# Optimization experiments

Measured on AMD Instinct MI355X. Metric: run time of the kernel, lower is better.

## Reference

```python
import jax, jax.numpy as jnp
import numpy as np

N = 40000; E = 400000; F = 16; H = 8; C = 64; R1 = 40; R2 = 40; MAXR = 60
NEG_SLOPE = 0.2


def setup_inputs() -> dict:
    key = jax.random.key(0)
    ks = jax.random.split(key, 16)
    inp = {}
    inp['x1'] = jax.random.normal(ks[0], (N, F), dtype=jnp.float32)
    inp['edge_index1'] = jax.random.randint(ks[1], (2, E), 0, N)
    inp['edge_attr1'] = jax.random.normal(ks[2], (E, 4), dtype=jnp.float32)
    inp['route_vec1'] = jax.random.randint(ks[3], (N,), 0, R1)
    inp['n_routes1'] = R1
    inp['x2'] = jax.random.normal(ks[4], (N, F), dtype=jnp.float32)
    inp['edge_index2'] = jax.random.randint(ks[5], (2, E), 0, N)
    inp['edge_attr2'] = jax.random.normal(ks[6], (E, 4), dtype=jnp.float32)
    inp['route_vec2'] = jax.random.randint(ks[7], (N,), 0, R2)
    inp['n_routes2'] = R2
    # GATConv params (glorot-ish scaling)
    inp['W_gat'] = jax.random.normal(ks[8], (F, H * C), dtype=jnp.float32) / np.sqrt(F)
    inp['att_src'] = jax.random.normal(ks[9], (H, C), dtype=jnp.float32) / np.sqrt(C)
    inp['att_dst'] = jax.random.normal(ks[10], (H, C), dtype=jnp.float32) / np.sqrt(C)
    inp['bias_gat'] = jnp.zeros((H * C,), dtype=jnp.float32)
    # route combination head: Linear(2*H*C -> MAXR+1)
    D = 2 * H * C
    inp['W_head'] = jax.random.normal(ks[11], (D, MAXR + 1), dtype=jnp.float32) / np.sqrt(D)
    inp['b_head'] = jnp.zeros((MAXR + 1,), dtype=jnp.float32)
    return inp


def _gat_conv(x, edge_index, W, att_src, att_dst, bias):
    """PyG GATConv (concat=True, add_self_loops=True, eval-mode dropout, edge_attr ignored)."""
    n = x.shape[0]
    loops = jnp.arange(n, dtype=edge_index.dtype)
    ei = jnp.concatenate([edge_index, jnp.stack([loops, loops])], axis=1)
    src, dst = ei[0], ei[1]
    h = (x @ W).reshape(n, H, C)                      # [N,H,C]
    a_s = jnp.sum(h * att_src, axis=-1)               # [N,H]
    a_d = jnp.sum(h * att_dst, axis=-1)               # [N,H]
    e = jax.nn.leaky_relu(a_s[src] + a_d[dst], NEG_SLOPE)   # [E',H]
    m = jax.ops.segment_max(e, dst, num_segments=n)   # stable softmax per dst node
    ex = jnp.exp(e - m[dst])
    denom = jax.ops.segment_sum(ex, dst, num_segments=n)
    alpha = ex / denom[dst]                           # [E',H]
    out = jax.ops.segment_sum(h[src] * alpha[:, :, None], dst, num_segments=n)  # [N,H,C]
    return out.reshape(n, H * C) + bias


def reference(x1, edge_index1, edge_attr1, route_vec1, n_routes1,
              x2, edge_index2, edge_attr2, route_vec2, n_routes2,
              W_gat, att_src, att_dst, bias_gat, W_head, b_head):
    # edge_attr is ignored: GATConv was built without edge_dim.
    emb1 = _gat_conv(x1, edge_index1, W_gat, att_src, att_dst, bias_gat)  # [N,H*C]
    emb2 = _gat_conv(x2, edge_index2, W_gat, att_src, att_dst, bias_gat)
    # one-hot(node->route).T @ emb  ==  segment_sum over routes
    agg1 = jax.ops.segment_sum(emb1, route_vec1, num_segments=n_routes1)  # [R1,H*C]
    agg2 = jax.ops.segment_sum(emb2, route_vec2, num_segments=n_routes2)  # [R2,H*C]
    a = jnp.broadcast_to(agg1[:, None, :], (n_routes1, n_routes2, H * C))
    b = jnp.broadcast_to(agg2[None, :, :], (n_routes1, n_routes2, H * C))
    pair = jnp.concatenate([a, b], axis=-1)                               # [R1,R2,2HC]
    full = pair @ W_head + b_head                                         # [R1,R2,MAXR+1]
    max_to_swap = min(n_routes1, n_routes2)
    logits = full[:n_routes1, :n_routes2, :max_to_swap - 1]
    probs = jax.nn.softmax(logits.reshape(-1), axis=-1).reshape(logits.shape)
    return probs
```

## Files before the change

kernel.cpp:

```cpp
#include <hip/hip_runtime.h>
#include <hip/hip_fp16.h>

#define NN 40000
#define NE 400000
#define NF 16
#define NH 8
#define NR 40
#define NK 39
#define NEG 0.2f
#define NBLK 157
#define NCH 16
#define NB 157
#define SLOT 3328
#define BPG2 196
#define GAB 40
#define WS 0.0625f

#define OFF_AS   0
#define OFF_AD   (OFF_AS + 2*NN*NH)
#define OFF_P    (OFF_AD + 2*NN*NH)
#define OFF_PART (OFF_P + 2*NR*NK)
#define OFF_S    (OFF_PART + 2*NR*NCH*128)
#define OFF_XH   (OFF_S + 2*NN*64)
#define OFF_INT  (OFF_XH + 2*NN*8)
#define IOFF_RHIST  0
#define IOFF_BCUR   (2*NR)
#define IOFF_RCUR   (2*NR + 2*NB)
#define IOFF_START  (IOFF_RCUR + 2*NR)
#define IOFF_DEG    (IOFF_START + 2*NN)
#define IOFF_NID    (IOFF_DEG + 2*NN)
#define IOFF_BINNED (IOFF_NID + 2*NN)
#define IOFF_SRC    (IOFF_BINNED + 2*NB*SLOT)

static __device__ __forceinline__ unsigned int f2bf(float v) {
    unsigned int x = __float_as_uint(v);
    return (x + 0x7FFFu + ((x >> 16) & 1u)) >> 16;
}
static __device__ __forceinline__ float bf2f(unsigned int u) {
    return __uint_as_float(u << 16);
}
static __device__ __forceinline__ unsigned int packh2(float a, float b) {
    __half2 hv = __floats2half2_rn(a, b);
    return *(unsigned int*)&hv;
}
static __device__ __forceinline__ float2 unpackh2(unsigned int u) {
    __half2 hv = *(__half2*)&u;
    return __half22float2(hv);
}

__global__ __launch_bounds__(512) void k_zero(int* __restrict__ p,
                                              int* __restrict__ srcs) {
    int i = threadIdx.x;
    if (i < 2 * NR + 2 * NB + 2 * NR) p[i] = 0;
    if (i == 0) srcs[2 * NB * SLOT] = 0;
}

__global__ __launch_bounds__(1024) void k_front(const float* __restrict__ x1,
                                                const float* __restrict__ x2,
                                                const int* __restrict__ rv1,
                                                const int* __restrict__ rv2,
                                                const int* __restrict__ ei1,
                                                const int* __restrict__ ei2,
                                                const float* __restrict__ W,
                                                const float* __restrict__ asrc,
                                                const float* __restrict__ adst,
                                                float* __restrict__ as_,
                                                float* __restrict__ ad_,
                                                unsigned int* __restrict__ xh,
                                                int* __restrict__ rhist,
                                                int* __restrict__ bcur,
                                                unsigned int* __restrict__ binned) {
    __shared__ float us[256];
    __shared__ int lh[NR];
    __shared__ int lhb[NB], lbb[NB];
    int tid = threadIdx.x;
    if (blockIdx.x < 2 * GAB) {
        if (tid < NR) lh[tid] = 0;
        if (tid < 256) {
            int tt = tid & 127;
            int f = tt >> 3, h = tt & 7;
            const float* av = (tid < 128 ? asrc : adst) + h * 64;
            const float* wrow = W + f * 512 + h * 64;
            float su = 0.f;
            for (int c = 0; c < 64; ++c) su += wrow[c] * av[c];
            us[tid] = su;
        }
        __syncthreads();
        int g = blockIdx.x / GAB;
        int n = (blockIdx.x - g * GAB) * 1024 + tid;
        if (n < NN) {
            const float* x = g ? x2 : x1;
            const int* rv = g ? rv2 : rv1;
            const float4* xp = (const float4*)(x + n * NF);
            float4 v0 = xp[0], v1 = xp[1], v2 = xp[2], v3 = xp[3];
            float xv[16] = {v0.x, v0.y, v0.z, v0.w, v1.x, v1.y, v1.z, v1.w,
                            v2.x, v2.y, v2.z, v2.w, v3.x, v3.y, v3.z, v3.w};
            int o = g * NN * NH + n * NH;
            for (int h = 0; h < NH; ++h) {
                float s1 = 0.f, s2 = 0.f;
                for (int f = 0; f < NF; ++f) {
                    s1 += xv[f] * us[f * 8 + h];
                    s2 += xv[f] * us[128 + f * 8 + h];
                }
                as_[o + h] = s1;
                ad_[o + h] = s2;
            }
            unsigned int* xo = xh + ((size_t)g * NN + n) * 8;
            #pragma unroll
            for (int p = 0; p < 8; ++p) xo[p] = packh2(xv[2 * p], xv[2 * p + 1]);
            atomicAdd(&lh[rv[n]], 1);
        }
        __syncthreads();
        if (tid < NR && lh[tid]) atomicAdd(&rhist[g * NR + tid], lh[tid]);
    } else {
        int bid = blockIdx.x - 2 * GAB;
        int g = bid >= BPG2;
        int blk = bid - g * BPG2;
        if (tid < NB) lhb[tid] = 0;
        __syncthreads();
        int e2 = blk * 1024 + tid;
        const int* ei = g ? ei2 : ei1;
        unsigned int v0 = 0, v1 = 0;
        int bin0 = 0, bin1 = 0, lp0 = 0, lp1 = 0;
        bool valid = (e2 < NE / 2);
        if (valid) {
            int2 sv = *(const int2*)&ei[2 * e2];
            int2 dv = *(const int2*)&ei[NE + 2 * e2];
            v0 = ((unsigned int)dv.x << 16) | (unsigned int)sv.x;
            v1 = ((unsigned int)dv.y << 16) | (unsigned int)sv.y;
            bin0 = (unsigned int)dv.x >> 8;
            bin1 = (unsigned int)dv.y >> 8;
            lp0 = atomicAdd(&lhb[bin0], 1);
            lp1 = atomicAdd(&lhb[bin1], 1);
        }
        __syncthreads();
        if (tid < NB && lhb[tid]) lbb[tid] = atomicAdd(&bcur[g * NB + tid], lhb[tid]);
        __syncthreads();
        if (valid) {
            int p0 = lbb[bin0] + lp0;
            int p1 = lbb[bin1] + lp1;
            if (p0 < SLOT) binned[(g * NB + bin0) * SLOT + p0] = v0;
            if (p1 < SLOT) binned[(g * NB + bin1) * SLOT + p1] = v1;
        }
    }
}

__global__ __launch_bounds__(256) void k_mid(const int* __restrict__ bcur,
                                             const unsigned int* __restrict__ binned,
                                             const int* __restrict__ rv1,
                                             const int* __restrict__ rv2,
                                             const int* __restrict__ rhist,
                                             int* __restrict__ rcur,
                                             int* __restrict__ start,
                                             int* __restrict__ deg,
                                             int* __restrict__ srcs,
                                             int* __restrict__ nid) {
    __shared__ unsigned int ed[SLOT];
    __shared__ int hist[256], scn[256];
    __shared__ int lh[NR], lbase[NR], rbase[NR];
    int tid = threadIdx.x;
    if (blockIdx.x < 2 * NB) {
        int gb = blockIdx.x;
        int g = gb >= NB;
        int b = gb - g * NB;
        int m = bcur[gb]; if (m > SLOT) m = SLOT;
        int base = gb * SLOT;
        for (int i = tid; i < m; i += 256) ed[i] = binned[base + i];
        hist[tid] = 0;
        __syncthreads();
        for (int i = tid; i < m; i += 256) atomicAdd(&hist[(ed[i] >> 16) & 255], 1);
        __syncthreads();
        int v = hist[tid];
        scn[tid] = v;
        __syncthreads();
        for (int off = 1; off < 256; off <<= 1) {
            int u = (tid >= off) ? scn[tid - off] : 0;
            __syncthreads();
            scn[tid] += u;
            __syncthreads();
        }
        int excl = scn[tid] - v;
        int d = b * 256 + tid;
        if (d < NN) { start[g * NN + d] = base + excl; deg[g * NN + d] = v; }
        hist[tid] = excl;
        __syncthreads();
        for (int i = tid; i < m; i += 256) {
            unsigned int e = ed[i];
            int ld = (e >> 16) & 255;
            int pos = atomicAdd(&hist[ld], 1);
            srcs[base + pos] = (int)(e & 0xffffu);
        }
    } else {
        int bid = blockIdx.x - 2 * NB;
        int g = bid / NBLK;
        int n = (bid - g * NBLK) * 256 + tid;
        const int* rv = g ? rv2 : rv1;
        if (tid < NR) lh[tid] = 0;
        __syncthreads();
        int r = 0, lpos = 0;
        bool valid = (n < NN);
        if (valid) { r = rv[n]; lpos = atomicAdd(&lh[r], 1); }
        if (tid == 0) {
            int run = 0;
            for (int rr = 0; rr < NR; ++rr) { rbase[rr] = run; run += rhist[g * NR + rr]; }
        }
        __syncthreads();
        if (tid < NR && lh[tid])
            lbase[tid] = rbase[tid] + atomicAdd(&rcur[g * NR + tid], lh[tid]);
        __syncthreads();
        if (valid) nid[g * NN + lbase[r] + lpos] = n;
    }
}

__global__ __launch_bounds__(256) void k_gather(const int* __restrict__ start,
                                                const int* __restrict__ deg,
                                                const int* __restrict__ srcs,
                                                const float* __restrict__ as_,
                                                const float* __restrict__ ad_,
                                                const unsigned int* __restrict__ xh,
                                                unsigned int* __restrict__ sb) {
    int bid = blockIdx.x;
    int xcd = bid & 7;
    int g = xcd >> 2;
    int lblk = (xcd & 3) * 2500 + (bid >> 3);
    int d = lblk * 4 + (threadIdx.x >> 6);
    int idx = g * NN + d;
    const float* asg = as_ + (size_t)g * NN * NH;
    const unsigned int* xg = xh + (size_t)g * NN * 8;
    int lane = threadIdx.x & 63;
    int h = lane >> 3, q = lane & 7;
    int a8 = lane >> 3;
    float adv = ad_[(size_t)g * NN * NH + d * NH + h];
    float e0 = asg[d * NH + h] + adv;
    e0 = (e0 > 0.f) ? e0 : NEG * e0;
    float w0 = __expf(e0) * WS;
    float2 xv = unpackh2(xg[d * 8 + q]);
    float wsum = w0;
    float ax = w0 * xv.x, ay = w0 * xv.y;
    int base = __builtin_amdgcn_readfirstlane(start[idx]);
    int dg   = __builtin_amdgcn_readfirstlane(deg[idx]);
    int nb = (dg + 7) >> 3;
    for (int b = 0; b < nb; ++b) {
        int off = base + b * 8;
        int lim = dg - b * 8;
        int aq = (q < lim) ? off + q : base;
        int aA = (a8 < lim) ? off + a8 : base;
        int sq = srcs[aq];
        int sA = srcs[aA];
        float ev = asg[sq * NH + h] + adv;
        ev = (ev > 0.f) ? ev : NEG * ev;
        float wq = (q < lim) ? __expf(ev) * WS : 0.f;
        float wpart = __shfl_xor(wq, 1);
        unsigned int wpair = (q & 1) ? packh2(wpart, wq) : packh2(wq, wpart);
        unsigned int xu = xg[sA * 8 + q];
        #pragma unroll
        for (int p = 0; p < 4; ++p) {
            unsigned int wp = (unsigned int)__shfl((int)wpair, (lane & 56) | (p << 1));
            float2 wf = unpackh2(wp);
            unsigned int xj0 = (unsigned int)__shfl((int)xu, ((p << 1) << 3) | q);
            unsigned int xj1 = (unsigned int)__shfl((int)xu, (((p << 1) | 1) << 3) | q);
            float2 x0 = unpackh2(xj0);
            float2 x1 = unpackh2(xj1);
            wsum += wf.x + wf.y;
            ax += wf.x * x0.x + wf.y * x1.x;
            ay += wf.x * x0.y + wf.y * x1.y;
        }
    }
    float inv = 1.0f / wsum;
    unsigned int pk = (f2bf(ay * inv) << 16) | f2bf(ax * inv);
    sb[(size_t)idx * 64 + lane] = pk;
}

__global__ __launch_bounds__(256) void k_rnode(const int* __restrict__ rhist,
                                               const int* __restrict__ nid,
                                               const unsigned int* __restrict__ sb,
                                               float* __restrict__ part) {
    __shared__ float red[4][128];
    __shared__ int sseg[2];
    int bid = blockIdx.x;
    int xcd = bid & 7;
    int g = xcd >> 2;
    int rch = (xcd & 3) * (NR * NCH / 4) + (bid >> 3);
    int r = rch / NCH, ch = rch - r * NCH;
    if (threadIdx.x == 0) {
        int acc = 0;
        for (int rr = 0; rr < r; ++rr) acc += rhist[g * NR + rr];
        sseg[0] = acc;
        sseg[1] = rhist[g * NR + r];
    }
    __syncthreads();
    int seg0 = sseg[0], dgr = sseg[1];
    int csz = (dgr + NCH - 1) / NCH;
    int a = seg0 + ch * csz;
    int b = seg0 + dgr; { int bb = a + csz; if (bb < b) b = bb; }
    int ln = threadIdx.x >> 6;
    int lane = threadIdx.x & 63;
    int par = lane >> 5;
    int p = lane & 31;
    const int* np = nid + g * NN;
    const unsigned int* sg = sb + (size_t)g * NN * 64;
    float sx0 = 0.f, sy0 = 0.f, sx1 = 0.f, sy1 = 0.f;
    for (int i = a + ln * 2 + par; i < b; i += 8) {
        int n = np[i];
        uint2 pk = *(const uint2*)&sg[(size_t)n * 64 + p * 2];
        sx0 += bf2f(pk.x & 0xffffu); sy0 += bf2f(pk.x >> 16);
        sx1 += bf2f(pk.y & 0xffffu); sy1 += bf2f(pk.y >> 16);
    }
    sx0 += __shfl_xor(sx0, 32);
    sy0 += __shfl_xor(sy0, 32);
    sx1 += __shfl_xor(sx1, 32);
    sy1 += __shfl_xor(sy1, 32);
    if (par == 0) {
        red[ln][p * 4 + 0] = sx0;
        red[ln][p * 4 + 1] = sy0;
        red[ln][p * 4 + 2] = sx1;
        red[ln][p * 4 + 3] = sy1;
    }
    __syncthreads();
    int tid = threadIdx.x;
    if (tid < 128) {
        float s = red[0][tid] + red[1][tid] + red[2][tid] + red[3][tid];
        part[((g * NR + r) * NCH + ch) * 128 + tid] = s;
    }
}

__global__ __launch_bounds__(256) void k_head(const float* __restrict__ part,
                                              const int* __restrict__ rhist,
                                              const float* __restrict__ W,
                                              const float* __restrict__ bias,
                                              const float* __restrict__ Wh,
                                              float* __restrict__ P) {
    __shared__ float trow[128];
    __shared__ float aggL[512];
    __shared__ float scnt;
    int g = blockIdx.x / NR, i = blockIdx.x - g * NR;
    int tid = threadIdx.x;
    if (tid < 128) {
        const float* pp = part + ((g * NR + i) * NCH) * 128 + tid;
        float s = 0.f;
        for (int ch = 0; ch < NCH; ++ch) s += pp[ch * 128];
        trow[tid] = s;
    }
    if (tid == 0) scnt = (float)rhist[g * NR + i];
    __syncthreads();
    for (int hc = tid; hc < 512; hc += 256) {
        int h = hc >> 6;
        float acc = scnt * bias[hc];
        const float* tp = trow + h * 16;
        for (int f = 0; f < 16; ++f) acc += tp[f] * W[f * 512 + hc];
        aggL[hc] = acc;
    }
    __syncthreads();
    if (tid < 4 * NK) {
        int k = tid >> 2, qq = tid & 3;
        const float* wp = Wh + (size_t)(g * 512 + qq * 128) * 61 + k;
        const float* ap = aggL + qq * 128;
        float acc = 0.f;
        for (int d = 0; d < 128; ++d) acc += ap[d] * wp[d * 61];
        acc += __shfl_down(acc, 1);
        acc += __shfl_down(acc, 2);
        if (qq == 0) P[(g * NR + i) * NK + k] = acc;
    }
}

__global__ __launch_bounds__(1024) void k_final(const float* __restrict__ P,
                                                const float* __restrict__ bh,
                                                float* __restrict__ out) {
    __shared__ float p1[NR * NK], p2[NR * NK];
    __shared__ float ak[NK], ck[NK], s1k[NK], s2k[NK];
    __shared__ float fk[NK];
    int tid = threadIdx.x;
    for (int i = tid; i < NR * NK; i += 1024) { p1[i] = P[i]; p2[i] = P[NR * NK + i]; }
    __syncthreads();
    if (tid < 2 * NK) {
        int k = (tid < NK) ? tid : tid - NK;
        float* pp = (tid < NK) ? p1 : p2;
        float a = -3.0e38f;
        for (int i = 0; i < NR; ++i) a = fmaxf(a, pp[i * NK + k]);
        float s = 0.f;
        for (int i = 0; i < NR; ++i) {
            float e = __expf(pp[i * NK + k] - a);
            pp[i * NK + k] = e;
            s += e;
        }
        if (tid < NK) { ak[k] = a; s1k[k] = s; }
        else          { ck[k] = a; s2k[k] = s; }
    }
    __syncthreads();
    if (tid == 0) {
        float M = -3.0e38f;
        float mk[NK];
        for (int k = 0; k < NK; ++k) {
            mk[k] = ak[k] + ck[k] + bh[k];
            M = fmaxf(M, mk[k]);
        }
        float den = 0.f;
        for (int k = 0; k < NK; ++k) den += s1k[k] * s2k[k] * __expf(mk[k] - M);
        float invden = 1.0f / den;
        for (int k = 0; k < NK; ++k) fk[k] = __expf(mk[k] - M) * invden;
    }
    __syncthreads();
    const int TOT = NR * NR * NK;
    for (int idx = tid; idx < TOT; idx += 1024) {
        int i = idx / (NR * NK);
        int r = idx - i * (NR * NK);
        int j = r / NK;
        int k = r - j * NK;
        out[idx] = p1[i * NK + k] * p2[j * NK + k] * fk[k];
    }
}

extern "C" void kernel_launch(void* const* d_in, const int* in_sizes, int n_in,
                              void* d_out, int out_size, void* d_ws, size_t ws_size,
                              hipStream_t stream) {
    const float* x1   = (const float*)d_in[0];
    const int*   ei1  = (const int*)d_in[1];
    const int*   rv1  = (const int*)d_in[3];
    const float* x2   = (const float*)d_in[5];
    const int*   ei2  = (const int*)d_in[6];
    const int*   rv2  = (const int*)d_in[8];
    const float* Wg   = (const float*)d_in[10];
    const float* asrc = (const float*)d_in[11];
    const float* adst = (const float*)d_in[12];
    const float* bias = (const float*)d_in[13];
    const float* Wh   = (const float*)d_in[14];
    const float* bh   = (const float*)d_in[15];
    float* out = (float*)d_out;
    float* ws  = (float*)d_ws;

    float* as_  = ws + OFF_AS;
    float* ad_  = ws + OFF_AD;
    float* P    = ws + OFF_P;
    float* part = ws + OFF_PART;
    unsigned int* sb = (unsigned int*)(ws + OFF_S);
    unsigned int* xh = (unsigned int*)(ws + OFF_XH);
    int* ibase  = (int*)(ws + OFF_INT);
    int* rhist  = ibase + IOFF_RHIST;
    int* bcur   = ibase + IOFF_BCUR;
    int* rcur   = ibase + IOFF_RCUR;
    int* start  = ibase + IOFF_START;
    int* deg    = ibase + IOFF_DEG;
    int* nid    = ibase + IOFF_NID;
    unsigned int* binned = (unsigned int*)(ibase + IOFF_BINNED);
    int* srcs   = ibase + IOFF_SRC;

    k_zero<<<1, 512, 0, stream>>>(rhist, srcs);
    k_front<<<2 * GAB + 2 * BPG2, 1024, 0, stream>>>(x1, x2, rv1, rv2, ei1, ei2,
                                                     Wg, asrc, adst, as_, ad_, xh,
                                                     rhist, bcur, binned);
    k_mid<<<2 * NB + 2 * NBLK, 256, 0, stream>>>(bcur, binned, rv1, rv2, rhist,
                                                 rcur, start, deg, srcs, nid);
    k_gather<<<2 * NN / 4, 256, 0, stream>>>(start, deg, srcs, as_, ad_, xh, sb);
    k_rnode<<<2 * NR * NCH, 256, 0, stream>>>(rhist, nid, sb, part);
    k_head<<<2 * NR, 256, 0, stream>>>(part, rhist, Wg, bias, Wh, P);
    k_final<<<1, 1024, 0, stream>>>(P, bh, out);
}
```

Measured before the change: 97.83 us.

## Sort destination nodes by in-degree before the gather to balance wavefront work

Builds a per-graph degree histogram in k_mid and adds a k_dsort kernel that counting-sorts nodes by in-degree into a permutation. k_gather then reads node ids through this permutation, so wavefronts in the same block handle nodes of similar degree. The aim is to cut divergence and tail imbalance in the per-edge loop. The cost is an extra kernel launch, an extra indirection, and less locality in the gather's writes and its reads of per-node data.

```diff
diff --git a/kernel.cpp b/kernel.cpp
--- a/kernel.cpp
+++ b/kernel.cpp
@@ -15,6 +15,7 @@
 #define BPG2 196
 #define GAB 40
 #define WS 0.0625f
+#define NDB 64
 
 #define OFF_AS   0
 #define OFF_AD   (OFF_AS + 2*NN*NH)
@@ -26,10 +27,14 @@
 #define IOFF_RHIST  0
 #define IOFF_BCUR   (2*NR)
 #define IOFF_RCUR   (2*NR + 2*NB)
-#define IOFF_START  (IOFF_RCUR + 2*NR)
+#define IOFF_DHIST  (IOFF_RCUR + 2*NR)
+#define IOFF_DCUR   (IOFF_DHIST + 2*NDB)
+#define NZERO       (IOFF_DCUR + 2*NDB)
+#define IOFF_START  NZERO
 #define IOFF_DEG    (IOFF_START + 2*NN)
 #define IOFF_NID    (IOFF_DEG + 2*NN)
-#define IOFF_BINNED (IOFF_NID + 2*NN)
+#define IOFF_DPERM  (IOFF_NID + 2*NN)
+#define IOFF_BINNED (IOFF_DPERM + 2*NN)
 #define IOFF_SRC    (IOFF_BINNED + 2*NB*SLOT)
 
 static __device__ __forceinline__ unsigned int f2bf(float v) {
@@ -48,10 +53,10 @@
     return __half22float2(hv);
 }
 
-__global__ __launch_bounds__(512) void k_zero(int* __restrict__ p,
-                                              int* __restrict__ srcs) {
+__global__ __launch_bounds__(1024) void k_zero(int* __restrict__ p,
+                                               int* __restrict__ srcs) {
     int i = threadIdx.x;
-    if (i < 2 * NR + 2 * NB + 2 * NR) p[i] = 0;
+    if (i < NZERO) p[i] = 0;
     if (i == 0) srcs[2 * NB * SLOT] = 0;
 }
 
@@ -154,10 +159,12 @@
                                              int* __restrict__ start,
                                              int* __restrict__ deg,
                                              int* __restrict__ srcs,
-                                             int* __restrict__ nid) {
+                                             int* __restrict__ nid,
+                                             int* __restrict__ dhist) {
     __shared__ unsigned int ed[SLOT];
     __shared__ int hist[256], scn[256];
     __shared__ int lh[NR], lbase[NR], rbase[NR];
+    __shared__ int dh[NDB];
     int tid = threadIdx.x;
     if (blockIdx.x < 2 * NB) {
         int gb = blockIdx.x;
@@ -167,6 +174,7 @@
         int base = gb * SLOT;
         for (int i = tid; i < m; i += 256) ed[i] = binned[base + i];
         hist[tid] = 0;
+        if (tid < NDB) dh[tid] = 0;
         __syncthreads();
         for (int i = tid; i < m; i += 256) atomicAdd(&hist[(ed[i] >> 16) & 255], 1);
         __syncthreads();
@@ -181,9 +189,14 @@
         }
         int excl = scn[tid] - v;
         int d = b * 256 + tid;
-        if (d < NN) { start[g * NN + d] = base + excl; deg[g * NN + d] = v; }
+        if (d < NN) {
+            start[g * NN + d] = base + excl;
+            deg[g * NN + d] = v;
+            atomicAdd(&dh[(v < NDB) ? v : (NDB - 1)], 1);
+        }
         hist[tid] = excl;
         __syncthreads();
+        if (tid < NDB && dh[tid]) atomicAdd(&dhist[g * NDB + tid], dh[tid]);
         for (int i = tid; i < m; i += 256) {
             unsigned int e = ed[i];
             int ld = (e >> 16) & 255;
@@ -212,18 +225,48 @@
     }
 }
 
+__global__ __launch_bounds__(256) void k_dsort(const int* __restrict__ deg,
+                                               const int* __restrict__ dhist,
+                                               int* __restrict__ dcur,
+                                               int* __restrict__ dperm) {
+    __shared__ int lh[NDB], lbase[NDB], dbase[NDB];
+    int tid = threadIdx.x;
+    int g = blockIdx.x / NBLK;
+    int n = (blockIdx.x - g * NBLK) * 256 + tid;
+    if (tid < NDB) lh[tid] = 0;
+    __syncthreads();
+    bool valid = (n < NN);
+    int bin = 0, lpos = 0;
+    if (valid) {
+        int v = deg[g * NN + n];
+        bin = (v < NDB) ? v : (NDB - 1);
+        lpos = atomicAdd(&lh[bin], 1);
+    }
+    if (tid == 0) {
+        int run = 0;
+        for (int b = 0; b < NDB; ++b) { dbase[b] = run; run += dhist[g * NDB + b]; }
+    }
+    __syncthreads();
+    if (tid < NDB && lh[tid])
+        lbase[tid] = dbase[tid] + atomicAdd(&dcur[g * NDB + tid], lh[tid]);
+    __syncthreads();
+    if (valid) dperm[g * NN + lbase[bin] + lpos] = n;
+}
+
 __global__ __launch_bounds__(256) void k_gather(const int* __restrict__ start,
                                                 const int* __restrict__ deg,
                                                 const int* __restrict__ srcs,
                                                 const float* __restrict__ as_,
                                                 const float* __restrict__ ad_,
                                                 const unsigned int* __restrict__ xh,
+                                                const int* __restrict__ dperm,
                                                 unsigned int* __restrict__ sb) {
     int bid = blockIdx.x;
     int xcd = bid & 7;
     int g = xcd >> 2;
     int lblk = (xcd & 3) * 2500 + (bid >> 3);
-    int d = lblk * 4 + (threadIdx.x >> 6);
+    int lidx = lblk * 4 + (threadIdx.x >> 6);
+    int d = dperm[g * NN + lidx];
     int idx = g * NN + d;
     const float* asg = as_ + (size_t)g * NN * NH;
     const unsigned int* xg = xh + (size_t)g * NN * 8;
@@ -438,19 +481,23 @@
     int* rhist  = ibase + IOFF_RHIST;
     int* bcur   = ibase + IOFF_BCUR;
     int* rcur   = ibase + IOFF_RCUR;
+    int* dhist  = ibase + IOFF_DHIST;
+    int* dcur   = ibase + IOFF_DCUR;
     int* start  = ibase + IOFF_START;
     int* deg    = ibase + IOFF_DEG;
     int* nid    = ibase + IOFF_NID;
+    int* dperm  = ibase + IOFF_DPERM;
     unsigned int* binned = (unsigned int*)(ibase + IOFF_BINNED);
     int* srcs   = ibase + IOFF_SRC;
 
-    k_zero<<<1, 512, 0, stream>>>(rhist, srcs);
+    k_zero<<<1, 1024, 0, stream>>>(rhist, srcs);
     k_front<<<2 * GAB + 2 * BPG2, 1024, 0, stream>>>(x1, x2, rv1, rv2, ei1, ei2,
                                                      Wg, asrc, adst, as_, ad_, xh,
                                                      rhist, bcur, binned);
     k_mid<<<2 * NB + 2 * NBLK, 256, 0, stream>>>(bcur, binned, rv1, rv2, rhist,
-                                                 rcur, start, deg, srcs, nid);
-    k_gather<<<2 * NN / 4, 256, 0, stream>>>(start, deg, srcs, as_, ad_, xh, sb);
+                                                 rcur, start, deg, srcs, nid, dhist);
+    k_dsort<<<2 * NBLK, 256, 0, stream>>>(deg, dhist, dcur, dperm);
+    k_gather<<<2 * NN / 4, 256, 0, stream>>>(start, deg, srcs, as_, ad_, xh, dperm, sb);
     k_rnode<<<2 * NR * NCH, 256, 0, stream>>>(rhist, nid, sb, part);
     k_head<<<2 * NR, 256, 0, stream>>>(part, rhist, Wg, bias, Wh, P);
     k_final<<<1, 1024, 0, stream>>>(P, bh, out);
```

After: 109.8 us. 12.2% more time.
